# Kernel optimization log

Measured on AMD Instinct MI355X. Metric: run time of the kernel, lower is better.

The kernel has to match this reference:

```python
import jax, jax.numpy as jnp
import numpy as np

BW = 2            # bit width
THR = 0.5         # brevitas TernaryQuant threshold
W_SCALE = 0.1     # SignedTernaryWeightPerTensorConst scale
A_SCALE = 1.0     # SignedTernaryActPerTensorConst scale


def _ste(x, q):
    # straight-through estimator: forward q, gradient identity
    return x + jax.lax.stop_gradient(q - x)


def ternary(x, scale):
    # brevitas TernaryQuant: {-scale, 0, +scale} with threshold*scale
    q = jnp.where(x > THR * scale, scale,
                  jnp.where(x < -THR * scale, -scale, 0.0)).astype(x.dtype)
    return _ste(x, q)


def fp_quant(w, bw=BW):
    # Int8WeightPerTensorFixedPoint at bw bits: power-of-two per-tensor scale
    int_max = 2.0 ** (bw - 1) - 1.0
    maxabs = jax.lax.stop_gradient(jnp.max(jnp.abs(w)))
    scale = 2.0 ** jnp.ceil(jnp.log2(maxabs / int_max))
    q = jnp.clip(jnp.round(w / scale), -(2.0 ** (bw - 1)), int_max) * scale
    return _ste(w, q)


def setup_inputs() -> dict:
    key = jax.random.key(0)
    ks = jax.random.split(key, 8)
    V, E, H, L, O = 30000, 1024, 1024, 2, 4
    B, T = 64, 512
    text = jax.random.randint(ks[0], (B, T), 0, V, dtype=jnp.int64)
    text_lengths = jax.random.randint(ks[1], (B,), 1, T, dtype=jnp.int64)
    s = 0.1
    emb_W = jax.random.normal(ks[2], (V, E), jnp.float32) * s
    W_ih = jax.random.normal(ks[3], (L, H, E), jnp.float32) * s
    W_hh = jax.random.normal(ks[4], (L, H, H), jnp.float32) * s
    b_ih = jax.random.normal(ks[5], (L, H), jnp.float32) * s
    b_hh = jax.random.normal(ks[6], (L, H), jnp.float32) * s
    fc_W = jax.random.normal(ks[7], (O, H), jnp.float32) * s
    return {"text": text, "text_lengths": text_lengths, "emb_W": emb_W,
            "W_ih": W_ih, "W_hh": W_hh, "b_ih": b_ih, "b_hh": b_hh,
            "fc_W": fc_W}


def reference(text, text_lengths, emb_W, W_ih, W_hh, b_ih, b_hh, fc_W):
    # quantized embedding lookup -> [B,T,E]
    x = fp_quant(emb_W)[text]
    x = ternary(x, A_SCALE)  # io_quant on RNN input
    n_layers = W_ih.shape[0]
    finals = []
    for l in range(n_layers):
        Wi = ternary(W_ih[l], W_SCALE)  # [H,in]
        Wh = ternary(W_hh[l], W_SCALE)  # [H,H]
        b = b_ih[l] + b_hh[l]
        # precompute input contribution for all timesteps: [B,T,H]
        xw = jnp.einsum('bte,he->bth', x, Wi) + b
        B = x.shape[0]
        h0 = jnp.zeros((B, Wh.shape[0]), x.dtype)

        def step(h, xw_t):
            acc = ternary(xw_t + h @ Wh.T, A_SCALE)   # gate_acc_quant
            h_new = ternary(jnp.tanh(acc), A_SCALE)   # tanh_quant / io_quant
            return h_new, h_new

        h_last, ys = jax.lax.scan(step, h0, jnp.swapaxes(xw, 0, 1))
        x = jnp.swapaxes(ys, 0, 1)  # [B,T,H] feeds next layer
        finals.append(h_last)
    hidden = jnp.stack(finals)  # [L,B,H] = hidden_state
    # quantized linear (no bias) applied to hidden_state -> [L,B,O]
    return jnp.einsum('lbh,oh->lbo', hidden, ternary(fc_W, W_SCALE))
```

## Files before the change

kernel.cpp:

```cpp
#include <hip/hip_runtime.h>
#include <cstdint>
#include <cstddef>


#define DRAIN_VMEM() asm volatile("s_waitcnt vmcnt(0)" ::: "memory")

static __device__ __forceinline__ float bf2f(unsigned short b) {
  return __uint_as_float(((unsigned)b) << 16);
}
static __device__ __forceinline__ unsigned short f2bf(float f) {
  unsigned u = __float_as_uint(f);
  u = (u + 0x7FFFu + ((u >> 16) & 1u)) >> 16;
  return (unsigned short)u;
}
static __device__ __forceinline__ float loadw(const void* p, size_t i, int isf32) {
  return isf32 ? ((const float*)p)[i] : bf2f(((const unsigned short*)p)[i]);
}

__global__ __launch_bounds__(256) void k_detect(const unsigned short* __restrict__ embu,
                                                const int* __restrict__ text,
                                                int* __restrict__ flags) {
  int i = blockIdx.x * 256 + threadIdx.x;
  unsigned e = (embu[i] >> 7) & 0xFFu;
  unsigned long long b = __ballot(e >= 127u);
  if ((threadIdx.x & 63) == 0 && b) atomicOr(&flags[0], 1);
  if (blockIdx.x == 0 && threadIdx.x == 0) {
    int allz = 1;
    for (int j = 0; j < 32; j++)
      if (text[2 * j + 1] != 0) allz = 0;
    flags[1] = allz;
  }
}

__global__ __launch_bounds__(256) void k_maxabs(const uint4* __restrict__ w,
                                                const int* __restrict__ flags,
                                                unsigned* __restrict__ out) {
  int isf32 = flags[0];
  int n16 = isf32 ? 7680000 : 3840000;
  float mf = 0.f;
  unsigned mb = 0;
  int i = blockIdx.x * blockDim.x + threadIdx.x;
  int stride = gridDim.x * blockDim.x;
  if (isf32) {
    for (; i < n16; i += stride) {
      uint4 v = w[i];
      mf = fmaxf(mf, fabsf(__uint_as_float(v.x)));
      mf = fmaxf(mf, fabsf(__uint_as_float(v.y)));
      mf = fmaxf(mf, fabsf(__uint_as_float(v.z)));
      mf = fmaxf(mf, fabsf(__uint_as_float(v.w)));
    }
  } else {
    for (; i < n16; i += stride) {
      uint4 v = w[i];
      unsigned a;
      a = v.x & 0x7FFF7FFFu; mb = max(mb, a & 0xFFFFu); mb = max(mb, a >> 16);
      a = v.y & 0x7FFF7FFFu; mb = max(mb, a & 0xFFFFu); mb = max(mb, a >> 16);
      a = v.z & 0x7FFF7FFFu; mb = max(mb, a & 0xFFFFu); mb = max(mb, a >> 16);
      a = v.w & 0x7FFF7FFFu; mb = max(mb, a & 0xFFFFu); mb = max(mb, a >> 16);
    }
    mf = bf2f((unsigned short)mb);
  }
  for (int off = 32; off > 0; off >>= 1) mf = fmaxf(mf, __shfl_down(mf, off));
  __shared__ float red[4];
  if ((threadIdx.x & 63) == 0) red[threadIdx.x >> 6] = mf;
  __syncthreads();
  if (threadIdx.x == 0) {
    float b = fmaxf(fmaxf(red[0], red[1]), fmaxf(red[2], red[3]));
    atomicMax(out, __float_as_uint(b));
  }
}

__global__ __launch_bounds__(1024) void k_tern_rows(
    const void* __restrict__ Wih, const void* __restrict__ Whh,
    const void* __restrict__ fcw, const int* __restrict__ flags,
    unsigned long long* __restrict__ wim, unsigned long long* __restrict__ whm,
    unsigned long long* __restrict__ fcm) {
  int isf32 = flags[0];
  int b = blockIdx.x;
  const void* src;
  size_t rowoff;
  unsigned long long* dst;
  if (b < 2048)      { src = Wih; rowoff = (size_t)b * 1024; dst = wim + (size_t)b * 32; }
  else if (b < 4096) { int r = b - 2048; src = Whh; rowoff = (size_t)r * 1024; dst = whm + (size_t)r * 32; }
  else               { int r = b - 4096; src = fcw; rowoff = (size_t)r * 1024; dst = fcm + (size_t)r * 32; }
  double w = (double)loadw(src, rowoff + threadIdx.x, isf32);
  unsigned long long bp = __ballot(w > 0.05);
  unsigned long long bm = __ballot(w < -0.05);
  if ((threadIdx.x & 63) == 0) {
    int wv = threadIdx.x >> 6;
    dst[2 * wv] = bp;
    dst[2 * wv + 1] = bp | bm;
  }
}

__global__ __launch_bounds__(1024) void k_embed(const int* __restrict__ text,
    const void* __restrict__ emb, const int* __restrict__ flags,
    const unsigned* __restrict__ mab, unsigned long long* __restrict__ x0) {
  int isf32 = flags[0], i64 = flags[1];
  int bt = blockIdx.x;
  long long tok = i64 ? ((const long long*)text)[bt] : (long long)text[bt];
  double ma = (double)__uint_as_float(*mab);
  float s = (float)exp2(ceil(log2(ma)));
  float inv_s = 1.0f / s;
  float w = loadw(emb, (size_t)tok * 1024 + threadIdx.x, isf32);
  float q = rintf(w * inv_s);
  q = fminf(fmaxf(q, -2.0f), 1.0f);
  float val = q * s;
  int code = (val > 0.5f) ? 1 : ((val < -0.5f) ? -1 : 0);
  unsigned long long bp = __ballot(code == 1);
  unsigned long long bm = __ballot(code == -1);
  if ((threadIdx.x & 63) == 0) {
    int wv = threadIdx.x >> 6;
    x0[(size_t)bt * 32 + 2 * wv] = bp;
    x0[(size_t)bt * 32 + 2 * wv + 1] = bp | bm;
  }
}

__global__ __launch_bounds__(256, 4) void k_bitgemm(const unsigned long long* __restrict__ xm,
    const unsigned long long* __restrict__ wim, short* __restrict__ nbuf) {
  __shared__ __align__(16) uint4 lx[64 * 16];
  __shared__ unsigned any[64];
  int tid = threadIdx.x;
  int bt0 = blockIdx.x * 64;
  int r = blockIdx.y * 256 + tid;
  unsigned wplo[16], wphi[16], wzlo[16], wzhi[16];
  const uint4* wrow = (const uint4*)(wim + (size_t)r * 32);
#pragma unroll
  for (int i = 0; i < 16; i++) {
    uint4 w4 = wrow[i];
    wplo[i] = w4.x; wphi[i] = w4.y; wzlo[i] = w4.z; wzhi[i] = w4.w;
  }
  if (tid < 64) any[tid] = 0;
  __syncthreads();
  unsigned accor = 0;
#pragma unroll
  for (int i = 0; i < 4; i++) {
    int idx = tid * 4 + i;
    uint4 v = ((const uint4*)(xm + (size_t)bt0 * 32))[idx];
    lx[idx] = v;
    accor |= v.z | v.w;
  }
  if (accor) atomicOr(&any[tid >> 2], 1u);
  __syncthreads();
  for (int bt = 0; bt < 64; bt++) {
    int k = 0;
    if (any[bt]) {
      const uint4* hx = lx + bt * 16;
      int sb = 0, sn = 0;
#pragma unroll
      for (int i = 0; i < 16; i++) {
        uint4 h = hx[i];
        unsigned blo = h.z & wzlo[i];
        unsigned bhi = h.w & wzhi[i];
        unsigned nlo = (h.x ^ wplo[i]) & blo;
        unsigned nhi = (h.y ^ wphi[i]) & bhi;
        sb += __popc(blo) + __popc(bhi);
        sn += __popc(nlo) + __popc(nhi);
      }
      k = sb - 2 * sn;
    }
    nbuf[(size_t)(bt0 + bt) * 1024 + r] = (short)k;
  }
}

#define FLAG_STRIDE 16

static __device__ __forceinline__ int ldflag(const int* p) {
  return __hip_atomic_load(p, __ATOMIC_RELAXED, __HIP_MEMORY_SCOPE_AGENT);
}
static __device__ __forceinline__ void stflag(int* p, int v) {
  __hip_atomic_store(p, v, __ATOMIC_RELAXED, __HIP_MEMORY_SCOPE_AGENT);
}

template <int ROLE>
static __device__ __forceinline__ void recur_stage(
    uint4 (*shb)[16], const short* nbuf,
    const unsigned long long* __restrict__ whm,
    const void* __restrict__ bih, const void* __restrict__ bhh,
    int isf32, int layer, int b, int r,
    unsigned long long* xrow,
    int* flagsA, int* flagsB,
    unsigned long long* __restrict__ hidm) {
  unsigned wplo[16], wphi[16], wzlo[16], wzhi[16];
  const uint4* wrow = (const uint4*)(whm + (size_t)(layer * 1024 + r) * 32);
#pragma unroll
  for (int i = 0; i < 16; i++) {
    uint4 w4 = wrow[i];
    wplo[i] = w4.x; wphi[i] = w4.y; wzlo[i] = w4.z; wzhi[i] = w4.w;
  }
  size_t boff = (size_t)layer * 1024 + r;
  double bias = (double)loadw(bih, boff, isf32) + (double)loadw(bhh, boff, isf32);
  int kp = (int)ceil((0.5 - bias) * 10.0);
  while ((double)kp * 0.1 + bias <= 0.5) kp++;
  while ((double)(kp - 1) * 0.1 + bias > 0.5) kp--;
  int km = (int)floor((-0.5 - bias) * 10.0);
  while ((double)km * 0.1 + bias >= -0.5) km--;
  while ((double)(km + 1) * 0.1 + bias < -0.5) km++;

  if (r < 32) ((unsigned long long*)shb)[r] = 0;
  const short* nrow = nbuf + (size_t)b * 512 * 1024 + r;
  int wv = r >> 6;
  bool l0 = (r & 63) == 0;
  int fl = 0;
  int nin;
  if (ROLE == 0) {
    nin = (int)nrow[0];
  } else {
    while ((fl = ldflag(flagsB + b * FLAG_STRIDE)) < 1) {}
    nin = (int)__hip_atomic_load(nrow, __ATOMIC_RELAXED, __HIP_MEMORY_SCOPE_AGENT);
  }
  __syncthreads();
  int pb = 0;
  unsigned long long plo = 0, phi = 0;
  for (int t = 0; t < 512; t++) {
    if (ROLE == 0) {
      if (l0 && t > 0) {
        __hip_atomic_store(xrow + (size_t)(t - 1) * 32 + 2 * wv, plo,
                           __ATOMIC_RELAXED, __HIP_MEMORY_SCOPE_AGENT);
        __hip_atomic_store(xrow + (size_t)(t - 1) * 32 + 2 * wv + 1, phi,
                           __ATOMIC_RELAXED, __HIP_MEMORY_SCOPE_AGENT);
      }
    } else {
      if (t < 511 && fl < t + 2)
        fl = ldflag(flagsB + b * FLAG_STRIDE);
    }
    const uint4* Hq = shb[pb];
    int sb = 0, sn = 0;
#pragma unroll
    for (int i = 0; i < 8; i++) {
      uint4 h = Hq[i];
      unsigned blo = h.z & wzlo[i];
      unsigned bhi = h.w & wzhi[i];
      unsigned nlo = (h.x ^ wplo[i]) & blo;
      unsigned nhi = (h.y ^ wphi[i]) & bhi;
      sb += __popc(blo) + __popc(bhi);
      sn += __popc(nlo) + __popc(nhi);
    }
    int nin_next = 0;
    bool got = true;
    if (ROLE == 0) {
      if (t < 511) nin_next = (int)nrow[(size_t)(t + 1) * 1024];
    } else if (t < 511) {
      got = (fl >= t + 2);
      if (got)
        nin_next = (int)__hip_atomic_load(nrow + (size_t)(t + 1) * 1024,
                                          __ATOMIC_RELAXED, __HIP_MEMORY_SCOPE_AGENT);
    }
#pragma unroll
    for (int i = 8; i < 16; i++) {
      uint4 h = Hq[i];
      unsigned blo = h.z & wzlo[i];
      unsigned bhi = h.w & wzhi[i];
      unsigned nlo = (h.x ^ wplo[i]) & blo;
      unsigned nhi = (h.y ^ wphi[i]) & bhi;
      sb += __popc(blo) + __popc(bhi);
      sn += __popc(nlo) + __popc(nhi);
    }
    int k = nin + sb - 2 * sn;
    unsigned long long bp = __ballot(k >= kp);
    unsigned long long bm = __ballot(k <= km);
    unsigned long long bz = bp | bm;
    if (l0) {
      uint4 o;
      o.x = (unsigned)bp; o.y = (unsigned)(bp >> 32);
      o.z = (unsigned)bz; o.w = (unsigned)(bz >> 32);
      shb[pb ^ 1][wv] = o;
      plo = bp; phi = bz;
    }
    if (ROLE == 2 && !got && t < 511) {
      while ((fl = ldflag(flagsB + b * FLAG_STRIDE)) < t + 2) {}
      nin_next = (int)__hip_atomic_load(nrow + (size_t)(t + 1) * 1024,
                                        __ATOMIC_RELAXED, __HIP_MEMORY_SCOPE_AGENT);
    }
    if (ROLE == 0) DRAIN_VMEM();
    __syncthreads();
    if (ROLE == 0 && r == 0 && t > 0)
      stflag(flagsA + b * FLAG_STRIDE, t);
    pb ^= 1;
    nin = nin_next;
  }
  if (ROLE == 0) {
    if (l0) {
      __hip_atomic_store(xrow + (size_t)511 * 32 + 2 * wv, plo,
                         __ATOMIC_RELAXED, __HIP_MEMORY_SCOPE_AGENT);
      __hip_atomic_store(xrow + (size_t)511 * 32 + 2 * wv + 1, phi,
                         __ATOMIC_RELAXED, __HIP_MEMORY_SCOPE_AGENT);
    }
    DRAIN_VMEM();
    __syncthreads();
    if (r == 0) stflag(flagsA + b * FLAG_STRIDE, 512);
  }
  if (r < 16) {
    uint4 h = shb[pb][r];
    size_t ho = (size_t)(layer * 64 + b) * 32;
    hidm[ho + 2 * r]     = ((unsigned long long)h.y << 32) | h.x;
    hidm[ho + 2 * r + 1] = ((unsigned long long)h.w << 32) | h.z;
  }
}

__global__ __launch_bounds__(1024, 4) void k_pipe(
    short* nbuf, unsigned long long* x0,
    const unsigned long long* __restrict__ wim,
    const unsigned long long* __restrict__ whm,
    const void* __restrict__ bih, const void* __restrict__ bhh,
    const int* __restrict__ flags, int* flagsA, int* flagsB,
    unsigned long long* __restrict__ hidm) {
  __shared__ __align__(16) uint4 shb[2][16];
  int role = blockIdx.x % 3;
  int b = blockIdx.x / 3;
  int r = threadIdx.x;
  int isf32 = flags[0];
  if (role == 0) {
    recur_stage<0>(shb, nbuf, whm, bih, bhh, isf32, 0, b, r,
                   x0 + (size_t)b * 512 * 32, flagsA, flagsB, hidm);
  } else if (role == 1) {
    unsigned wplo[16], wphi[16], wzlo[16], wzhi[16];
    const uint4* wrow = (const uint4*)(wim + (size_t)(1024 + r) * 32);
#pragma unroll
    for (int i = 0; i < 16; i++) {
      uint4 w4 = wrow[i];
      wplo[i] = w4.x; wphi[i] = w4.y; wzlo[i] = w4.z; wzhi[i] = w4.w;
    }
    const unsigned long long* xsrc = x0 + (size_t)b * 512 * 32;
    short* nout = nbuf + (size_t)b * 512 * 1024 + r;
    int fa = 0;
    unsigned long long vcur = 0;
    if (r < 32) {
      while ((fa = ldflag(flagsA + b * FLAG_STRIDE)) < 1) {}
      vcur = __hip_atomic_load(xsrc + r, __ATOMIC_RELAXED, __HIP_MEMORY_SCOPE_AGENT);
    }
    for (int t = 0; t < 512; t++) {
      if (r < 32) ((unsigned long long*)(shb[t & 1]))[r] = vcur;
      __syncthreads();
      bool got = false;
      unsigned long long vnext = 0;
      if (r < 32 && t < 511) {
        if (fa < t + 2) fa = ldflag(flagsA + b * FLAG_STRIDE);
        if (fa >= t + 2) {
          vnext = __hip_atomic_load(xsrc + (size_t)(t + 1) * 32 + r,
                                    __ATOMIC_RELAXED, __HIP_MEMORY_SCOPE_AGENT);
          got = true;
        }
      }
      const uint4* hx = shb[t & 1];
      int sb = 0, sn = 0;
#pragma unroll
      for (int i = 0; i < 16; i++) {
        uint4 h = hx[i];
        unsigned blo = h.z & wzlo[i];
        unsigned bhi = h.w & wzhi[i];
        unsigned nlo = (h.x ^ wplo[i]) & blo;
        unsigned nhi = (h.y ^ wphi[i]) & bhi;
        sb += __popc(blo) + __popc(bhi);
        sn += __popc(nlo) + __popc(nhi);
      }
      __hip_atomic_store(nout + (size_t)t * 1024, (short)(sb - 2 * sn),
                         __ATOMIC_RELAXED, __HIP_MEMORY_SCOPE_AGENT);
      if (r < 32 && t < 511 && !got) {
        while ((fa = ldflag(flagsA + b * FLAG_STRIDE)) < t + 2) {}
        vnext = __hip_atomic_load(xsrc + (size_t)(t + 1) * 32 + r,
                                  __ATOMIC_RELAXED, __HIP_MEMORY_SCOPE_AGENT);
      }
      DRAIN_VMEM();
      __syncthreads();
      if (r == 0) stflag(flagsB + b * FLAG_STRIDE, t + 1);
      vcur = vnext;
    }
  } else {
    recur_stage<2>(shb, nbuf, whm, bih, bhh, isf32, 1, b, r,
                   (unsigned long long*)0, flagsA, flagsB, hidm);
  }
}

__global__ __launch_bounds__(64) void k_fc(const unsigned long long* __restrict__ hidm,
    const unsigned long long* __restrict__ fcm, const int* __restrict__ flags,
    void* __restrict__ out) {
  int isf32 = flags[0];
  int lb = blockIdx.x, lane = threadIdx.x;
  unsigned long long hp = 0, hz = 0;
  if (lane < 16) {
    hp = hidm[lb * 32 + 2 * lane];
    hz = hidm[lb * 32 + 2 * lane + 1];
  }
#pragma unroll
  for (int o = 0; o < 4; o++) {
    int k = 0;
    if (lane < 16) {
      unsigned long long wp = fcm[o * 32 + 2 * lane], wz = fcm[o * 32 + 2 * lane + 1];
      unsigned long long both = hz & wz;
      unsigned long long neg = both & (hp ^ wp);
      k = __popcll(both) - 2 * __popcll(neg);
    }
    for (int off = 8; off > 0; off >>= 1) k += __shfl_down(k, off);
    if (lane == 0) {
      float v = (float)((double)k * 0.1);
      if (isf32) ((float*)out)[lb * 4 + o] = v;
      else       ((unsigned short*)out)[lb * 4 + o] = f2bf(v);
    }
  }
}

extern "C" void kernel_launch(void* const* d_in, const int* in_sizes, int n_in,
                              void* d_out, int out_size, void* d_ws, size_t ws_size,
                              hipStream_t stream) {
  (void)in_sizes; (void)n_in; (void)out_size; (void)ws_size;
  const int* text = (const int*)d_in[0];
  const void* emb = d_in[2];
  const void* Wih = d_in[3];
  const void* Whh = d_in[4];
  const void* bih = d_in[5];
  const void* bhh = d_in[6];
  const void* fcw = d_in[7];

  char* ws = (char*)d_ws;
  int* flags = (int*)(ws);
  unsigned* mab = (unsigned*)(ws + 64);
  int* flagsA = (int*)(ws + 1024);
  int* flagsB = (int*)(ws + 5120);
  size_t off = 16384;
  unsigned long long* x0 = (unsigned long long*)(ws + off);  off += (size_t)32768 * 256;
  unsigned long long* wim = (unsigned long long*)(ws + off); off += (size_t)2048 * 256;
  unsigned long long* whm = (unsigned long long*)(ws + off); off += (size_t)2048 * 256;
  unsigned long long* fcm = (unsigned long long*)(ws + off); off += (size_t)4 * 256;
  unsigned long long* hidm = (unsigned long long*)(ws + off); off += (size_t)128 * 256;
  short* nbuf = (short*)(ws + off);                          off += (size_t)32768 * 1024 * 2;

  hipMemsetAsync(ws, 0, 16384, stream);
  k_detect<<<256, 256, 0, stream>>>((const unsigned short*)emb, text, flags);
  k_maxabs<<<2048, 256, 0, stream>>>((const uint4*)emb, flags, mab);
  k_tern_rows<<<4100, 1024, 0, stream>>>(Wih, Whh, fcw, flags, wim, whm, fcm);
  k_embed<<<32768, 1024, 0, stream>>>(text, emb, flags, mab, x0);
  k_bitgemm<<<dim3(512, 4), 256, 0, stream>>>(x0, wim, nbuf);
  k_pipe<<<192, 1024, 0, stream>>>(nbuf, x0, wim, whm, bih, bhh, flags,
                                   flagsA, flagsB, hidm);
  k_fc<<<128, 64, 0, stream>>>(hidm, fcm, flags, d_out);
}
```

Baseline: 1.509 ms.

## Broadcast hidden bits via readlane and deepen layer-1 input pipeline by one step

```diff
diff --git a/kernel.cpp b/kernel.cpp
--- a/kernel.cpp
+++ b/kernel.cpp
@@ -4,6 +4,7 @@
 
 
 #define DRAIN_VMEM() asm volatile("s_waitcnt vmcnt(0)" ::: "memory")
+#define FLAG_STRIDE 16
 
 static __device__ __forceinline__ float bf2f(unsigned short b) {
   return __uint_as_float(((unsigned)b) << 16);
@@ -163,7 +164,6 @@
   }
 }
 
-#define FLAG_STRIDE 16
 
 static __device__ __forceinline__ int ldflag(const int* p) {
   return __hip_atomic_load(p, __ATOMIC_RELAXED, __HIP_MEMORY_SCOPE_AGENT);
@@ -171,6 +171,21 @@
 static __device__ __forceinline__ void stflag(int* p, int v) {
   __hip_atomic_store(p, v, __ATOMIC_RELAXED, __HIP_MEMORY_SCOPE_AGENT);
 }
+
+#define DOT8(hq, I0, sb, sn)                                            \
+  _Pragma("unroll")                                                     \
+  for (int i = (I0); i < (I0) + 8; i++) {                               \
+    unsigned hx = (unsigned)__builtin_amdgcn_readlane((int)(hq).x, i);  \
+    unsigned hy = (unsigned)__builtin_amdgcn_readlane((int)(hq).y, i);  \
+    unsigned hz = (unsigned)__builtin_amdgcn_readlane((int)(hq).z, i);  \
+    unsigned hw = (unsigned)__builtin_amdgcn_readlane((int)(hq).w, i);  \
+    unsigned blo = hz & wzlo[i];                                        \
+    unsigned bhi = hw & wzhi[i];                                        \
+    unsigned nlo = (hx ^ wplo[i]) & blo;                                \
+    unsigned nhi = (hy ^ wphi[i]) & bhi;                                \
+    sb += __popc(blo) + __popc(bhi);                                    \
+    sn += __popc(nlo) + __popc(nhi);                                    \
+  }
 
 template <int ROLE>
 static __device__ __forceinline__ void recur_stage(
@@ -200,7 +215,8 @@
   if (r < 32) ((unsigned long long*)shb)[r] = 0;
   const short* nrow = nbuf + (size_t)b * 512 * 1024 + r;
   int wv = r >> 6;
-  bool l0 = (r & 63) == 0;
+  int lane = r & 63;
+  bool l0 = lane == 0;
   int fl = 0;
   int nin;
   if (ROLE == 0) {
@@ -224,18 +240,9 @@
       if (t < 511 && fl < t + 2)
         fl = ldflag(flagsB + b * FLAG_STRIDE);
     }
-    const uint4* Hq = shb[pb];
+    uint4 hq = shb[pb][lane & 15];
     int sb = 0, sn = 0;
-#pragma unroll
-    for (int i = 0; i < 8; i++) {
-      uint4 h = Hq[i];
-      unsigned blo = h.z & wzlo[i];
-      unsigned bhi = h.w & wzhi[i];
-      unsigned nlo = (h.x ^ wplo[i]) & blo;
-      unsigned nhi = (h.y ^ wphi[i]) & bhi;
-      sb += __popc(blo) + __popc(bhi);
-      sn += __popc(nlo) + __popc(nhi);
-    }
+    DOT8(hq, 0, sb, sn);
     int nin_next = 0;
     bool got = true;
     if (ROLE == 0) {
@@ -246,16 +253,7 @@
         nin_next = (int)__hip_atomic_load(nrow + (size_t)(t + 1) * 1024,
                                           __ATOMIC_RELAXED, __HIP_MEMORY_SCOPE_AGENT);
     }
-#pragma unroll
-    for (int i = 8; i < 16; i++) {
-      uint4 h = Hq[i];
-      unsigned blo = h.z & wzlo[i];
-      unsigned bhi = h.w & wzhi[i];
-      unsigned nlo = (h.x ^ wplo[i]) & blo;
-      unsigned nhi = (h.y ^ wphi[i]) & bhi;
-      sb += __popc(blo) + __popc(bhi);
-      sn += __popc(nlo) + __popc(nhi);
-    }
+    DOT8(hq, 8, sb, sn);
     int k = nin + sb - 2 * sn;
     unsigned long long bp = __ballot(k >= kp);
     unsigned long long bm = __ballot(k <= km);
@@ -323,49 +321,55 @@
     }
     const unsigned long long* xsrc = x0 + (size_t)b * 512 * 32;
     short* nout = nbuf + (size_t)b * 512 * 1024 + r;
+    int lane = r & 63;
     int fa = 0;
-    unsigned long long vcur = 0;
+    unsigned long long vnext = 0;
     if (r < 32) {
       while ((fa = ldflag(flagsA + b * FLAG_STRIDE)) < 1) {}
-      vcur = __hip_atomic_load(xsrc + r, __ATOMIC_RELAXED, __HIP_MEMORY_SCOPE_AGENT);
-    }
+      unsigned long long v0 = __hip_atomic_load(xsrc + r, __ATOMIC_RELAXED,
+                                                __HIP_MEMORY_SCOPE_AGENT);
+      ((unsigned long long*)(shb[0]))[r] = v0;
+      while (fa < 2) { fa = ldflag(flagsA + b * FLAG_STRIDE); }
+      vnext = __hip_atomic_load(xsrc + 32 + r, __ATOMIC_RELAXED,
+                                __HIP_MEMORY_SCOPE_AGENT);
+    }
+    __syncthreads();
+    short ncur = 0;
     for (int t = 0; t < 512; t++) {
-      if (r < 32) ((unsigned long long*)(shb[t & 1]))[r] = vcur;
-      __syncthreads();
+      if (r < 32 && t < 511) ((unsigned long long*)(shb[(t + 1) & 1]))[r] = vnext;
+      if (t > 0)
+        __hip_atomic_store(nout + (size_t)(t - 1) * 1024, ncur,
+                           __ATOMIC_RELAXED, __HIP_MEMORY_SCOPE_AGENT);
       bool got = false;
-      unsigned long long vnext = 0;
-      if (r < 32 && t < 511) {
-        if (fa < t + 2) fa = ldflag(flagsA + b * FLAG_STRIDE);
-        if (fa >= t + 2) {
-          vnext = __hip_atomic_load(xsrc + (size_t)(t + 1) * 32 + r,
-                                    __ATOMIC_RELAXED, __HIP_MEMORY_SCOPE_AGENT);
+      unsigned long long v2 = 0;
+      if (r < 32 && t < 510) {
+        if (fa < t + 3) fa = ldflag(flagsA + b * FLAG_STRIDE);
+        if (fa >= t + 3) {
+          v2 = __hip_atomic_load(xsrc + (size_t)(t + 2) * 32 + r,
+                                 __ATOMIC_RELAXED, __HIP_MEMORY_SCOPE_AGENT);
           got = true;
         }
       }
-      const uint4* hx = shb[t & 1];
+      uint4 hq = shb[t & 1][lane & 15];
       int sb = 0, sn = 0;
-#pragma unroll
-      for (int i = 0; i < 16; i++) {
-        uint4 h = hx[i];
-        unsigned blo = h.z & wzlo[i];
-        unsigned bhi = h.w & wzhi[i];
-        unsigned nlo = (h.x ^ wplo[i]) & blo;
-        unsigned nhi = (h.y ^ wphi[i]) & bhi;
-        sb += __popc(blo) + __popc(bhi);
-        sn += __popc(nlo) + __popc(nhi);
-      }
-      __hip_atomic_store(nout + (size_t)t * 1024, (short)(sb - 2 * sn),
-                         __ATOMIC_RELAXED, __HIP_MEMORY_SCOPE_AGENT);
-      if (r < 32 && t < 511 && !got) {
-        while ((fa = ldflag(flagsA + b * FLAG_STRIDE)) < t + 2) {}
-        vnext = __hip_atomic_load(xsrc + (size_t)(t + 1) * 32 + r,
-                                  __ATOMIC_RELAXED, __HIP_MEMORY_SCOPE_AGENT);
+      DOT8(hq, 0, sb, sn);
+      DOT8(hq, 8, sb, sn);
+      if (r < 32 && t < 510 && !got) {
+        while ((fa = ldflag(flagsA + b * FLAG_STRIDE)) < t + 3) {}
+        v2 = __hip_atomic_load(xsrc + (size_t)(t + 2) * 32 + r,
+                               __ATOMIC_RELAXED, __HIP_MEMORY_SCOPE_AGENT);
       }
       DRAIN_VMEM();
       __syncthreads();
-      if (r == 0) stflag(flagsB + b * FLAG_STRIDE, t + 1);
-      vcur = vnext;
-    }
+      if (r == 0 && t > 0) stflag(flagsB + b * FLAG_STRIDE, t);
+      ncur = (short)(sb - 2 * sn);
+      vnext = v2;
+    }
+    __hip_atomic_store(nout + (size_t)511 * 1024, ncur,
+                       __ATOMIC_RELAXED, __HIP_MEMORY_SCOPE_AGENT);
+    DRAIN_VMEM();
+    __syncthreads();
+    if (r == 0) stflag(flagsB + b * FLAG_STRIDE, 512);
   } else {
     recur_stage<2>(shb, nbuf, whm, bih, bhh, isf32, 1, b, r,
                    (unsigned long long*)0, flagsA, flagsB, hidm);
```

Result: no change. 1.514 ms (+0.4%).
